# Optimization experiments

Measured on AMD Instinct MI355X. Metric: run time of the kernel, lower is better.

Reference implementation:

```python
import jax, jax.numpy as jnp
import numpy as np

B, T, H, W, C_IN = 2, 12, 80, 120, 6
F = 32  # filters
KH = KW = 3


def _conv(x, w):
    # x: (N,H,W,Cin), w: (kh,kw,Cin,Cout), SAME padding, stride 1
    return jax.lax.conv_general_dilated(
        x, w, window_strides=(1, 1), padding='SAME',
        dimension_numbers=('NHWC', 'HWIO', 'NHWC'))


def _convgru_direction(x, Wx, b, Wh_zr, Wh_h, reverse):
    """ConvGRU2D over time. x: (B,T,H,W,Cin). Returns (B,T,H,W,F)."""
    Bn, Tn, Hn, Wn, Cn = x.shape
    Fn = Wh_h.shape[-1]
    # Input convolutions for all timesteps at once (time folded into batch).
    xc = _conv(x.reshape(Bn * Tn, Hn, Wn, Cn), Wx) + b          # (B*T,H,W,3F)
    xc = xc.reshape(Bn, Tn, Hn, Wn, 3 * Fn).transpose(1, 0, 2, 3, 4)  # (T,B,H,W,3F)
    h0 = jnp.zeros((Bn, Hn, Wn, Fn), x.dtype)

    def step(h, xt):
        xz, xr, xh = jnp.split(xt, 3, axis=-1)
        hz, hr = jnp.split(_conv(h, Wh_zr), 2, axis=-1)
        z = jax.nn.sigmoid(xz + hz)              # update gate
        r = jax.nn.sigmoid(xr + hr)              # reset gate
        hh = jnp.tanh(xh + _conv(r * h, Wh_h))   # candidate state
        h_new = z * h + (1.0 - z) * hh           # keras GRU update convention
        return h_new, h_new

    _, ys = jax.lax.scan(step, h0, xc, reverse=reverse)  # ys aligned with input time order
    return ys.transpose(1, 0, 2, 3, 4)  # (B,T,H,W,F)


def setup_inputs() -> dict:
    key = jax.random.key(0)
    ks = jax.random.split(key, 9)
    sx = 1.0 / np.sqrt(KH * KW * C_IN)
    sh = 1.0 / np.sqrt(KH * KW * F)
    return {
        'x': jax.random.normal(ks[0], (B, T, H, W, C_IN), jnp.float32),
        'Wx_f': jax.random.normal(ks[1], (KH, KW, C_IN, 3 * F), jnp.float32) * sx,
        'b_f': jnp.zeros((3 * F,), jnp.float32),
        'Wh_zr_f': jax.random.normal(ks[2], (KH, KW, F, 2 * F), jnp.float32) * sh,
        'Wh_h_f': jax.random.normal(ks[3], (KH, KW, F, F), jnp.float32) * sh,
        'Wx_b': jax.random.normal(ks[4], (KH, KW, C_IN, 3 * F), jnp.float32) * sx,
        'b_b': jnp.zeros((3 * F,), jnp.float32),
        'Wh_zr_b': jax.random.normal(ks[5], (KH, KW, F, 2 * F), jnp.float32) * sh,
        'Wh_h_b': jax.random.normal(ks[6], (KH, KW, F, F), jnp.float32) * sh,
    }


def reference(x, Wx_f, b_f, Wh_zr_f, Wh_h_f, Wx_b, b_b, Wh_zr_b, Wh_h_b):
    hs_f = _convgru_direction(x, Wx_f, b_f, Wh_zr_f, Wh_h_f, reverse=False)
    hs_b = _convgru_direction(x, Wx_b, b_b, Wh_zr_b, Wh_h_b, reverse=True)
    # Bidirectional(merge_mode=None) -> concat on channel axis (module's call)
    return jnp.concatenate([hs_f, hs_b], axis=-1)  # (B,T,H,W,2F)
```

## Files before the change

### kernel.cpp

```cpp
#include <hip/hip_runtime.h>
#include <hip/hip_bf16.h>

#define Bn 2
#define Tn 12
#define Hn 80
#define Wn 120
#define CIN 6
#define SITES (Hn * Wn)
#define HSZ (4 * SITES * 32)
#define GRID 512
#define BLK 256

#define NA_D (48 * 64 * 8)
#define NB_D (24 * 64 * 8)
#define NA (2 * NA_D)
#define NB (2 * NB_D)
#define NPX (Bn * Tn * SITES)
#define PREP_TOT (NA + NB + NPX)

#define ZSTR 34

typedef __attribute__((ext_vector_type(8))) short short8;
typedef __attribute__((ext_vector_type(4))) float f32x4;

__device__ __forceinline__ short f2bf(float f) {
    union { __hip_bfloat16 h; short s; } u;
    u.h = __float2bfloat16(f);
    return u.s;
}
__device__ __forceinline__ float bf2f(short s) {
    union { float f; unsigned u; } u;
    u.u = ((unsigned)(unsigned short)s) << 16;
    return u.f;
}
__device__ __forceinline__ float fast_sigmoid(float v) {
    return __builtin_amdgcn_rcpf(1.f + __expf(-v));
}
__device__ __forceinline__ float fast_tanh(float v) {
    v = fminf(fmaxf(v, -15.f), 15.f);
    float e = __expf(2.f * v);
    return (e - 1.f) * __builtin_amdgcn_rcpf(e + 1.f);
}

__device__ __forceinline__ short8 h_load16(const short* p) {
    union { unsigned long long q[2]; short8 v; } u;
    u.q[0] = __hip_atomic_load((const unsigned long long*)p,
                               __ATOMIC_RELAXED, __HIP_MEMORY_SCOPE_AGENT);
    u.q[1] = __hip_atomic_load((const unsigned long long*)(p + 4),
                               __ATOMIC_RELAXED, __HIP_MEMORY_SCOPE_AGENT);
    return u.v;
}
__device__ __forceinline__ void h_store16(short* p, short8 v) {
    union { short8 v; unsigned long long q[2]; } u; u.v = v;
    __hip_atomic_store((unsigned long long*)p, u.q[0],
                       __ATOMIC_RELAXED, __HIP_MEMORY_SCOPE_AGENT);
    __hip_atomic_store((unsigned long long*)(p + 4), u.q[1],
                       __ATOMIC_RELAXED, __HIP_MEMORY_SCOPE_AGENT);
}

__device__ __forceinline__ int swz16(int i) { return i ^ (((i >> 5) & 7) << 3); }

__global__ __launch_bounds__(BLK) void prep_kernel(
    const float* __restrict__ Wzr_f, const float* __restrict__ Wzr_b,
    const float* __restrict__ Wh_f,  const float* __restrict__ Wh_b,
    const float* __restrict__ Wx_f,  const float* __restrict__ Wx_b,
    const float* __restrict__ x,
    short* __restrict__ bopA, short* __restrict__ bopB, short* __restrict__ xb8,
    unsigned* __restrict__ flags)
{
    int i = blockIdx.x * BLK + threadIdx.x;
    if (i < GRID) flags[i << 5] = 0;
    if (i < NA) {
        int dir = i / NA_D; int r = i % NA_D;
        int f = r / 512; int lane = (r % 512) / 8; int j = r % 8;
        int q = lane >> 4, n = lane & 15;
        int chunk = f >> 2, nt = f & 3;
        float v = 0.f;
        if (chunk < 3) {
            int tap = chunk * 4 + q;
            if (tap < 9 && j < 6) v = (dir ? Wx_b : Wx_f)[(tap * CIN + j) * 96 + nt * 16 + n];
        } else {
            int tap = chunk - 3;
            v = (dir ? Wzr_b : Wzr_f)[(tap * 32 + q * 8 + j) * 64 + nt * 16 + n];
        }
        bopA[i] = f2bf(v);
    } else if (i < NA + NB) {
        int ii = i - NA;
        int dir = ii / NB_D; int r = ii % NB_D;
        int f = r / 512; int lane = (r % 512) / 8; int j = r % 8;
        int q = lane >> 4, n = lane & 15;
        int chunk = f >> 1, ntc = f & 1;
        float v = 0.f;
        if (chunk < 3) {
            int tap = chunk * 4 + q;
            if (tap < 9 && j < 6) v = (dir ? Wx_b : Wx_f)[(tap * CIN + j) * 96 + 64 + ntc * 16 + n];
        } else {
            int tap = chunk - 3;
            v = (dir ? Wh_b : Wh_f)[(tap * 32 + q * 8 + j) * 32 + ntc * 16 + n];
        }
        bopB[ii] = f2bf(v);
    } else if (i < PREP_TOT) {
        int p = i - NA - NB;
        const float* xp = x + (size_t)p * CIN;
        short v[8];
        #pragma unroll
        for (int c = 0; c < CIN; c++) v[c] = f2bf(xp[c]);
        v[6] = 0; v[7] = 0;
        *(short8*)&xb8[(size_t)p * 8] = *(short8*)v;
    }
}

__global__ __launch_bounds__(BLK, 2) void step_all(
    const short* __restrict__ xb8,
    const short* __restrict__ bopA, const short* __restrict__ bopB,
    const float* __restrict__ b_f, const float* __restrict__ b_b,
    short* __restrict__ hb0, short* __restrict__ hb1,
    float* __restrict__ out, unsigned* __restrict__ flags)
{
    __shared__ __align__(16) short bA_l[NA_D];
    __shared__ __align__(16) short rh_l[126 * 40];
    __shared__ __align__(16) float z_l[80 * ZSTR];
    __shared__ __align__(16) short h_l[9 * 20 * 32];

    int tid = threadIdx.x, bid = blockIdx.x;
    int seg = bid & 7;
    int t1  = bid >> 3;
    int yb  = t1 & 15;
    int field = t1 >> 4;
    int dir = field >> 1, b = field & 1;
    int y0 = yb * 5, x0 = seg * 16;

    {
        const short* src = bopA + dir * NA_D;
        #pragma unroll
        for (int it = 0; it < NA_D / (BLK * 8); it++) {
            int i = (it * BLK + tid) * 8;
            *(short8*)&bA_l[i] = *(const short8*)&src[i];
        }
    }
    for (int c = tid; c < 720; c += BLK) *(short8*)&h_l[c * 8] = (short8)(short)0;

    const short* bB   = bopB + dir * NB_D;
    const float* bias = dir ? b_b : b_f;
    short* hfield0 = hb0 + (size_t)field * SITES * 32;
    short* hfield1 = hb1 + (size_t)field * SITES * 32;

    int wid = tid >> 6, lane = tid & 63;
    int n = lane & 15, q = lane >> 4, q8 = q * 8;

    unsigned* myflag = flags + (bid << 5);
    const unsigned* nflag = nullptr;
    if (tid < 8) {
        int k = tid + (tid >= 4);
        int ny = yb + k / 3 - 1, nx = seg + k % 3 - 1;
        if (ny >= 0 && ny < 16 && nx >= 0 && nx < 8)
            nflag = flags + ((unsigned)((field << 7) | (ny << 3) | nx) << 5);
    }

    int  r_gofs[2], r_lofs[2];
    bool r_img[2];
    #pragma unroll
    for (int k = 0; k < 2; k++) {
        int u = tid + k * BLK;
        r_img[k] = false; r_gofs[k] = 0; r_lofs[k] = 0;
        if (u < 400) {
            int su = u >> 2, q4 = u & 3;
            int R, C;
            if (su < 80) { int rb = su / 20; R = (rb < 2) ? rb : rb + 5; C = su % 20; }
            else { int e = su - 80; R = 2 + (e >> 2); int ci = e & 3; C = (ci < 2) ? ci : ci + 16; }
            int gy = y0 - 2 + R, gx = x0 - 2 + C;
            r_lofs[k] = swz16((R * 20 + C) * 32 + q4 * 8);
            if (gy >= 0 && gy < Hn && gx >= 0 && gx < Wn) {
                r_img[k] = true;
                r_gofs[k] = (gy * Wn + gx) * 32 + q4 * 8;
            }
        }
    }

    int hs0 = (wid * 2) * 16 + n, hs1 = hs0 + 16;
    bool av0 = hs0 < 126, av1 = hs1 < 126;
    int hr0 = hs0 / 18, hc0 = hs0 - hr0 * 18;
    int hr1 = hs1 / 18, hc1 = hs1 - hr1 * 18;
    int gy0 = y0 - 1 + hr0, gx0 = x0 - 1 + hc0;
    int gy1 = y0 - 1 + hr1, gx1 = x0 - 1 + hc1;

    int  xaofs[2][3]; bool xaok[2][3];
    #pragma unroll
    for (int c = 0; c < 3; c++) {
        int tap = c * 4 + q;
        #pragma unroll
        for (int k = 0; k < 2; k++) { xaok[k][c] = false; xaofs[k][c] = 0; }
        if (tap < 9) {
            int dy = tap / 3 - 1, dx = tap % 3 - 1;
            int ay0 = gy0 + dy, ax0 = gx0 + dx;
            int ay1 = gy1 + dy, ax1 = gx1 + dx;
            if (av0 && ay0 >= 0 && ay0 < Hn && ax0 >= 0 && ax0 < Wn) {
                xaok[0][c] = true; xaofs[0][c] = (ay0 * Wn + ax0) * 8;
            }
            if (av1 && ay1 >= 0 && ay1 < Hn && ax1 >= 0 && ax1 < Wn) {
                xaok[1][c] = true; xaofs[1][c] = (ay1 * Wn + ax1) * 8;
            }
        }
    }
    int hofs0[9], hofs1[9];
    {
        int hbase0 = ((hr0 + 1) * 20 + hc0 + 1) * 32 + q8;
        int hbase1 = ((hr1 + 1) * 20 + hc1 + 1) * 32 + q8;
        #pragma unroll
        for (int tap = 0; tap < 9; tap++) {
            int d = ((tap / 3 - 1) * 20 + (tap % 3 - 1)) * 32;
            hofs0[tap] = swz16(hbase0 + d);
            hofs1[tap] = swz16(hbase1 + d);
        }
    }

    int t0 = wid * 2;
    bool v0 = (t0 < 5), v1 = (t0 + 1 < 5);
    int tc0 = t0, tc1 = v1 ? t0 + 1 : t0;
    int yB0 = y0 + tc0, yB1 = y0 + tc1;

    int  xbofs[2][3]; bool xbok[2][3];
    #pragma unroll
    for (int c = 0; c < 3; c++) {
        int tap = c * 4 + q;
        #pragma unroll
        for (int k = 0; k < 2; k++) { xbok[k][c] = false; xbofs[k][c] = 0; }
        if (tap < 9) {
            int dy = tap / 3 - 1, dx = tap % 3 - 1;
            int ax = x0 + n + dx;
            int ay0 = yB0 + dy, ay1 = yB1 + dy;
            if (ay0 >= 0 && ay0 < Hn && ax >= 0 && ax < Wn) {
                xbok[0][c] = true; xbofs[0][c] = (ay0 * Wn + ax) * 8;
            }
            if (ay1 >= 0 && ay1 < Hn && ax >= 0 && ax < Wn) {
                xbok[1][c] = true; xbofs[1][c] = (ay1 * Wn + ax) * 8;
            }
        }
    }
    int rofs0[9], rofs1[9];
    #pragma unroll
    for (int tap = 0; tap < 9; tap++) {
        int ky = tap / 3, kx = tap % 3;
        rofs0[tap] = ((tc0 + ky) * 18 + n + kx) * 40 + q8;
        rofs1[tap] = ((tc1 + ky) * 18 + n + kx) * 40 + q8;
    }

    float bvA[4], bvB2[2];
    #pragma unroll
    for (int nt = 0; nt < 4; nt++) bvA[nt] = bias[nt * 16 + n];
    #pragma unroll
    for (int c = 0; c < 2; c++) bvB2[c] = bias[64 + c * 16 + n];

    f32x4 hst[2][2];
    #pragma unroll
    for (int a = 0; a < 2; a++)
        #pragma unroll
        for (int c = 0; c < 2; c++) hst[a][c] = (f32x4)0.f;

    float* hpub = z_l;

    __syncthreads();

    #pragma unroll 1
    for (int s = 0; s < Tn; s++) {
        int t = dir ? (Tn - 1 - s) : s;
        const short* xs   = xb8 + (size_t)((b * Tn + t) * SITES) * 8;
        const short* hbpf = (s & 1) ? hfield0 : hfield1;
        short*       hbcf = (s & 1) ? hfield1 : hfield0;

        short8 xa[2][3];
        #pragma unroll
        for (int c = 0; c < 3; c++) {
            xa[0][c] = xaok[0][c] ? *(const short8*)&xs[xaofs[0][c]] : (short8)(short)0;
            xa[1][c] = xaok[1][c] ? *(const short8*)&xs[xaofs[1][c]] : (short8)(short)0;
        }

        if (s > 0) {
            if (nflag) {
                unsigned spins = 0;
                while (__hip_atomic_load(nflag, __ATOMIC_RELAXED, __HIP_MEMORY_SCOPE_AGENT)
                       < (unsigned)s) {
                    __builtin_amdgcn_s_sleep(1);
                    if (++spins > (1u << 22)) break;
                }
            }
            __syncthreads();
        }

        short8 rv0 = (short8)(short)0, rv1 = (short8)(short)0;
        if (s > 0) {
            if (r_img[0]) rv0 = h_load16(&hbpf[r_gofs[0]]);
            if (r_img[1]) rv1 = h_load16(&hbpf[r_gofs[1]]);
        }

        f32x4 acc[2][4];
        #pragma unroll
        for (int nt = 0; nt < 4; nt++) {
            acc[0][nt] = (f32x4)bvA[nt]; acc[1][nt] = (f32x4)bvA[nt];
        }
        #pragma unroll
        for (int c = 0; c < 3; c++) {
            #pragma unroll
            for (int nt = 0; nt < 4; nt++) {
                short8 Bf = *(const short8*)&bA_l[((c * 4 + nt) * 64 + lane) * 8];
                acc[0][nt] = __builtin_amdgcn_mfma_f32_16x16x32_bf16(xa[0][c], Bf, acc[0][nt], 0, 0, 0);
                acc[1][nt] = __builtin_amdgcn_mfma_f32_16x16x32_bf16(xa[1][c], Bf, acc[1][nt], 0, 0, 0);
            }
        }

        if (s > 0) {
            if (r_img[0]) *(short8*)&h_l[r_lofs[0]] = rv0;
            if (r_img[1]) *(short8*)&h_l[r_lofs[1]] = rv1;
        }
        __syncthreads();

        if (s > 0) {
            __builtin_amdgcn_s_setprio(1);
            #pragma unroll
            for (int tap = 0; tap < 9; tap++) {
                short8 a0 = *(const short8*)&h_l[hofs0[tap]];
                short8 a1 = *(const short8*)&h_l[hofs1[tap]];
                #pragma unroll
                for (int nt = 0; nt < 4; nt++) {
                    short8 Bf = *(const short8*)&bA_l[(((tap + 3) * 4 + nt) * 64 + lane) * 8];
                    acc[0][nt] = __builtin_amdgcn_mfma_f32_16x16x32_bf16(a0, Bf, acc[0][nt], 0, 0, 0);
                    acc[1][nt] = __builtin_amdgcn_mfma_f32_16x16x32_bf16(a1, Bf, acc[1][nt], 0, 0, 0);
                }
            }
            __builtin_amdgcn_s_setprio(0);
        }

        #pragma unroll
        for (int tl = 0; tl < 2; tl++) {
            int ht = wid * 2 + tl;
            #pragma unroll
            for (int r = 0; r < 4; r++) {
                int hs_e = ht * 16 + q * 4 + r;
                if (hs_e >= 126) continue;
                int hr_e = hs_e / 18, hc_e = hs_e - hr_e * 18;
                bool inter = (hr_e >= 1 && hr_e <= 5 && hc_e >= 1 && hc_e <= 16);
                int gy_e = y0 - 1 + hr_e, gx_e = x0 - 1 + hc_e;
                bool img = (gy_e >= 0 && gy_e < Hn && gx_e >= 0 && gx_e < Wn);
                #pragma unroll
                for (int nt = 0; nt < 2; nt++) {
                    if (img && inter)
                        z_l[((hr_e - 1) * 16 + hc_e - 1) * ZSTR + nt * 16 + n] =
                            fast_sigmoid(acc[tl][nt][r]);
                }
                #pragma unroll
                for (int nt = 2; nt < 4; nt++) {
                    int ch = (nt - 2) * 16 + n;
                    float hv = bf2f(h_l[swz16(((hr_e + 1) * 20 + hc_e + 1) * 32 + ch)]);
                    float rhv = fast_sigmoid(acc[tl][nt][r]) * hv;
                    rh_l[hs_e * 40 + ch] = f2bf(rhv);
                }
            }
        }
        __syncthreads();

        f32x4 acc2[2][2];
        if (v0) {
            #pragma unroll
            for (int ntc = 0; ntc < 2; ntc++) {
                acc2[0][ntc] = (f32x4)bvB2[ntc]; acc2[1][ntc] = (f32x4)bvB2[ntc];
            }
            __builtin_amdgcn_s_setprio(1);
            #pragma unroll
            for (int chunk = 0; chunk < 12; chunk++) {
                short8 a0, a1;
                if (chunk < 3) {
                    a0 = xbok[0][chunk] ? *(const short8*)&xs[xbofs[0][chunk]] : (short8)(short)0;
                    a1 = xbok[1][chunk] ? *(const short8*)&xs[xbofs[1][chunk]] : (short8)(short)0;
                } else {
                    a0 = *(const short8*)&rh_l[rofs0[chunk - 3]];
                    a1 = *(const short8*)&rh_l[rofs1[chunk - 3]];
                }
                #pragma unroll
                for (int ntc = 0; ntc < 2; ntc++) {
                    short8 Bf = *(const short8*)&bB[((chunk * 2 + ntc) * 64 + lane) * 8];
                    acc2[0][ntc] = __builtin_amdgcn_mfma_f32_16x16x32_bf16(a0, Bf, acc2[0][ntc], 0, 0, 0);
                    acc2[1][ntc] = __builtin_amdgcn_mfma_f32_16x16x32_bf16(a1, Bf, acc2[1][ntc], 0, 0, 0);
                }
            }
            __builtin_amdgcn_s_setprio(0);
        }
        __syncthreads();

        if (v0) {
            #pragma unroll
            for (int tl = 0; tl < 2; tl++) {
                if (tl == 1 && !v1) continue;
                int ti = t0 + tl;
                #pragma unroll
                for (int ntc = 0; ntc < 2; ntc++) {
                    f32x4 hp = hst[tl][ntc];
                    f32x4 hn;
                    #pragma unroll
                    for (int r = 0; r < 4; r++) {
                        int slot = (ti * 16 + q * 4 + r) * ZSTR + ntc * 16 + n;
                        float z  = z_l[slot];
                        float hh = fast_tanh(acc2[tl][ntc][r]);
                        hn[r] = z * hp[r] + (1.f - z) * hh;
                        hpub[slot] = hn[r];
                    }
                    hst[tl][ntc] = hn;
                }
            }
        }
        __syncthreads();

        if (s + 1 < Tn) {
            #pragma unroll
            for (int j = 0; j < 2; j++) {
                int u = tid + j * BLK;
                if (u < 320) {
                    int us = u >> 2, up = u & 3;
                    int row = us >> 4, col = us & 15;
                    int gx = x0 + col;
                    if (gx < Wn) {
                        short8 hv8;
                        #pragma unroll
                        for (int e = 0; e < 8; e++)
                            hv8[e] = f2bf(hpub[us * ZSTR + up * 8 + e]);
                        *(short8*)&h_l[swz16(((row + 2) * 20 + col + 2) * 32 + up * 8)] = hv8;
                        h_store16(&hbcf[(size_t)((y0 + row) * Wn + gx) * 32 + up * 8], hv8);
                    }
                }
            }
            asm volatile("s_waitcnt vmcnt(0)" ::: "memory");
            __syncthreads();
            if (tid == 0)
                __hip_atomic_store(myflag, (unsigned)(s + 1),
                                   __ATOMIC_RELAXED, __HIP_MEMORY_SCOPE_AGENT);
        }

        {
            size_t outb = (size_t)((b * Tn + t) * SITES) * 64 + dir * 32;
            #pragma unroll
            for (int j = 0; j < 3; j++) {
                int u = tid + j * BLK;
                if (u < 640) {
                    int us = u >> 3, up = u & 7;
                    int row = us >> 4, col = us & 15;
                    int gx = x0 + col;
                    if (gx < Wn) {
                        f32x4 v;
                        #pragma unroll
                        for (int e = 0; e < 4; e++)
                            v[e] = hpub[us * ZSTR + up * 4 + e];
                        __builtin_nontemporal_store(v,
                            (f32x4*)&out[outb + (size_t)((y0 + row) * Wn + gx) * 64 + up * 4]);
                    }
                }
            }
        }
    }
}

extern "C" void kernel_launch(void* const* d_in, const int* in_sizes, int n_in,
                              void* d_out, int out_size, void* d_ws, size_t ws_size,
                              hipStream_t stream)
{
    const float* x     = (const float*)d_in[0];
    const float* Wx_f  = (const float*)d_in[1];
    const float* b_f   = (const float*)d_in[2];
    const float* Wzr_f = (const float*)d_in[3];
    const float* Wh_f  = (const float*)d_in[4];
    const float* Wx_b  = (const float*)d_in[5];
    const float* b_b   = (const float*)d_in[6];
    const float* Wzr_b = (const float*)d_in[7];
    const float* Wh_b  = (const float*)d_in[8];
    float* out = (float*)d_out;

    char* w = (char*)d_ws;
    short* hb0  = (short*)w;  w += (size_t)HSZ * 2;
    short* hb1  = (short*)w;  w += (size_t)HSZ * 2;
    short* xb8  = (short*)w;  w += (size_t)NPX * 8 * 2;
    short* bopA = (short*)w;  w += (size_t)NA * 2;
    short* bopB = (short*)w;  w += (size_t)NB * 2;
    unsigned* flags = (unsigned*)w; w += (size_t)GRID * 32 * 4;

    prep_kernel<<<(PREP_TOT + BLK - 1) / BLK, BLK, 0, stream>>>(
        Wzr_f, Wzr_b, Wh_f, Wh_b, Wx_f, Wx_b, x, bopA, bopB, xb8, flags);

    step_all<<<GRID, BLK, 0, stream>>>(xb8, bopA, bopB, b_f, b_b,
                                       hb0, hb1, out, flags);
}
```

Baseline: 219.4 us.

## Double block size so each wave handles one M-tile instead of two

The persistent step kernel now runs with 512 threads (8 waves) per block instead of 256. Each wave computes one 16-row MFMA tile rather than two, which halves per-thread accumulators and address arrays. The candidate-state update is folded into the same phase as its GEMM, removing one barrier per timestep. This gives more waves per CU to hide latency and shortens each wave's serial MFMA chain, at the cost of barriers across more waves and fewer active waves in the 5-tile candidate phase (3 of 8 idle).

```diff
diff --git a/kernel.cpp b/kernel.cpp
--- a/kernel.cpp
+++ b/kernel.cpp
@@ -9,7 +9,8 @@
 #define SITES (Hn * Wn)
 #define HSZ (4 * SITES * 32)
 #define GRID 512
-#define BLK 256
+#define BLK 512
+#define PBLK 256
 
 #define NA_D (48 * 64 * 8)
 #define NB_D (24 * 64 * 8)
@@ -60,7 +61,7 @@
 
 __device__ __forceinline__ int swz16(int i) { return i ^ (((i >> 5) & 7) << 3); }
 
-__global__ __launch_bounds__(BLK) void prep_kernel(
+__global__ __launch_bounds__(PBLK) void prep_kernel(
     const float* __restrict__ Wzr_f, const float* __restrict__ Wzr_b,
     const float* __restrict__ Wh_f,  const float* __restrict__ Wh_b,
     const float* __restrict__ Wx_f,  const float* __restrict__ Wx_b,
@@ -68,7 +69,7 @@
     short* __restrict__ bopA, short* __restrict__ bopB, short* __restrict__ xb8,
     unsigned* __restrict__ flags)
 {
-    int i = blockIdx.x * BLK + threadIdx.x;
+    int i = blockIdx.x * PBLK + threadIdx.x;
     if (i < GRID) flags[i << 5] = 0;
     if (i < NA) {
         int dir = i / NA_D; int r = i % NA_D;
@@ -110,7 +111,7 @@
     }
 }
 
-__global__ __launch_bounds__(BLK, 2) void step_all(
+__global__ __launch_bounds__(BLK, 4) void step_all(
     const short* __restrict__ xb8,
     const short* __restrict__ bopA, const short* __restrict__ bopB,
     const float* __restrict__ b_f, const float* __restrict__ b_b,
@@ -157,92 +158,70 @@
             nflag = flags + ((unsigned)((field << 7) | (ny << 3) | nx) << 5);
     }
 
-    int  r_gofs[2], r_lofs[2];
-    bool r_img[2];
-    #pragma unroll
-    for (int k = 0; k < 2; k++) {
-        int u = tid + k * BLK;
-        r_img[k] = false; r_gofs[k] = 0; r_lofs[k] = 0;
-        if (u < 400) {
-            int su = u >> 2, q4 = u & 3;
-            int R, C;
-            if (su < 80) { int rb = su / 20; R = (rb < 2) ? rb : rb + 5; C = su % 20; }
-            else { int e = su - 80; R = 2 + (e >> 2); int ci = e & 3; C = (ci < 2) ? ci : ci + 16; }
-            int gy = y0 - 2 + R, gx = x0 - 2 + C;
-            r_lofs[k] = swz16((R * 20 + C) * 32 + q4 * 8);
-            if (gy >= 0 && gy < Hn && gx >= 0 && gx < Wn) {
-                r_img[k] = true;
-                r_gofs[k] = (gy * Wn + gx) * 32 + q4 * 8;
-            }
-        }
-    }
-
-    int hs0 = (wid * 2) * 16 + n, hs1 = hs0 + 16;
-    bool av0 = hs0 < 126, av1 = hs1 < 126;
-    int hr0 = hs0 / 18, hc0 = hs0 - hr0 * 18;
-    int hr1 = hs1 / 18, hc1 = hs1 - hr1 * 18;
-    int gy0 = y0 - 1 + hr0, gx0 = x0 - 1 + hc0;
-    int gy1 = y0 - 1 + hr1, gx1 = x0 - 1 + hc1;
-
-    int  xaofs[2][3]; bool xaok[2][3];
+    int  r_gofs = 0, r_lofs = 0;
+    bool r_img = false, r_unit = (tid < 400);
+    if (r_unit) {
+        int su = tid >> 2, q4 = tid & 3;
+        int R, C;
+        if (su < 80) { int rb = su / 20; R = (rb < 2) ? rb : rb + 5; C = su % 20; }
+        else { int e = su - 80; R = 2 + (e >> 2); int ci = e & 3; C = (ci < 2) ? ci : ci + 16; }
+        int gy = y0 - 2 + R, gx = x0 - 2 + C;
+        r_lofs = swz16((R * 20 + C) * 32 + q4 * 8);
+        if (gy >= 0 && gy < Hn && gx >= 0 && gx < Wn) {
+            r_img = true;
+            r_gofs = (gy * Wn + gx) * 32 + q4 * 8;
+        }
+    }
+
+    int hs = wid * 16 + n;
+    bool av = hs < 126;
+    int hr = hs / 18, hc = hs - hr * 18;
+    int gy = y0 - 1 + hr, gx = x0 - 1 + hc;
+
+    int  xaofs[3]; bool xaok[3];
     #pragma unroll
     for (int c = 0; c < 3; c++) {
         int tap = c * 4 + q;
-        #pragma unroll
-        for (int k = 0; k < 2; k++) { xaok[k][c] = false; xaofs[k][c] = 0; }
+        xaok[c] = false; xaofs[c] = 0;
         if (tap < 9) {
             int dy = tap / 3 - 1, dx = tap % 3 - 1;
-            int ay0 = gy0 + dy, ax0 = gx0 + dx;
-            int ay1 = gy1 + dy, ax1 = gx1 + dx;
-            if (av0 && ay0 >= 0 && ay0 < Hn && ax0 >= 0 && ax0 < Wn) {
-                xaok[0][c] = true; xaofs[0][c] = (ay0 * Wn + ax0) * 8;
-            }
-            if (av1 && ay1 >= 0 && ay1 < Hn && ax1 >= 0 && ax1 < Wn) {
-                xaok[1][c] = true; xaofs[1][c] = (ay1 * Wn + ax1) * 8;
-            }
-        }
-    }
-    int hofs0[9], hofs1[9];
+            int ay = gy + dy, ax = gx + dx;
+            if (av && ay >= 0 && ay < Hn && ax >= 0 && ax < Wn) {
+                xaok[c] = true; xaofs[c] = (ay * Wn + ax) * 8;
+            }
+        }
+    }
+    int hofs[9];
     {
-        int hbase0 = ((hr0 + 1) * 20 + hc0 + 1) * 32 + q8;
-        int hbase1 = ((hr1 + 1) * 20 + hc1 + 1) * 32 + q8;
-        #pragma unroll
-        for (int tap = 0; tap < 9; tap++) {
-            int d = ((tap / 3 - 1) * 20 + (tap % 3 - 1)) * 32;
-            hofs0[tap] = swz16(hbase0 + d);
-            hofs1[tap] = swz16(hbase1 + d);
-        }
-    }
-
-    int t0 = wid * 2;
-    bool v0 = (t0 < 5), v1 = (t0 + 1 < 5);
-    int tc0 = t0, tc1 = v1 ? t0 + 1 : t0;
-    int yB0 = y0 + tc0, yB1 = y0 + tc1;
-
-    int  xbofs[2][3]; bool xbok[2][3];
+        int hbase = ((hr + 1) * 20 + hc + 1) * 32 + q8;
+        #pragma unroll
+        for (int tap = 0; tap < 9; tap++)
+            hofs[tap] = swz16(hbase + ((tap / 3 - 1) * 20 + (tap % 3 - 1)) * 32);
+    }
+
+    bool vB = (wid < 5);
+    int ti = vB ? wid : 0;
+    int yB = y0 + ti;
+
+    int  xbofs[3]; bool xbok[3];
     #pragma unroll
     for (int c = 0; c < 3; c++) {
         int tap = c * 4 + q;
-        #pragma unroll
-        for (int k = 0; k < 2; k++) { xbok[k][c] = false; xbofs[k][c] = 0; }
+        xbok[c] = false; xbofs[c] = 0;
         if (tap < 9) {
             int dy = tap / 3 - 1, dx = tap % 3 - 1;
             int ax = x0 + n + dx;
-            int ay0 = yB0 + dy, ay1 = yB1 + dy;
-            if (ay0 >= 0 && ay0 < Hn && ax >= 0 && ax < Wn) {
-                xbok[0][c] = true; xbofs[0][c] = (ay0 * Wn + ax) * 8;
-            }
-            if (ay1 >= 0 && ay1 < Hn && ax >= 0 && ax < Wn) {
-                xbok[1][c] = true; xbofs[1][c] = (ay1 * Wn + ax) * 8;
-            }
-        }
-    }
-    int rofs0[9], rofs1[9];
+            int ay = yB + dy;
+            if (ay >= 0 && ay < Hn && ax >= 0 && ax < Wn) {
+                xbok[c] = true; xbofs[c] = (ay * Wn + ax) * 8;
+            }
+        }
+    }
+    int rofs[9];
     #pragma unroll
     for (int tap = 0; tap < 9; tap++) {
         int ky = tap / 3, kx = tap % 3;
-        rofs0[tap] = ((tc0 + ky) * 18 + n + kx) * 40 + q8;
-        rofs1[tap] = ((tc1 + ky) * 18 + n + kx) * 40 + q8;
+        rofs[tap] = ((ti + ky) * 18 + n + kx) * 40 + q8;
     }
 
     float bvA[4], bvB2[2];
@@ -251,11 +230,8 @@
     #pragma unroll
     for (int c = 0; c < 2; c++) bvB2[c] = bias[64 + c * 16 + n];
 
-    f32x4 hst[2][2];
-    #pragma unroll
-    for (int a = 0; a < 2; a++)
-        #pragma unroll
-        for (int c = 0; c < 2; c++) hst[a][c] = (f32x4)0.f;
+    f32x4 hst[2];
+    hst[0] = (f32x4)0.f; hst[1] = (f32x4)0.f;
 
     float* hpub = z_l;
 
@@ -268,12 +244,10 @@
         const short* hbpf = (s & 1) ? hfield0 : hfield1;
         short*       hbcf = (s & 1) ? hfield1 : hfield0;
 
-        short8 xa[2][3];
-        #pragma unroll
-        for (int c = 0; c < 3; c++) {
-            xa[0][c] = xaok[0][c] ? *(const short8*)&xs[xaofs[0][c]] : (short8)(short)0;
-            xa[1][c] = xaok[1][c] ? *(const short8*)&xs[xaofs[1][c]] : (short8)(short)0;
-        }
+        short8 xa[3];
+        #pragma unroll
+        for (int c = 0; c < 3; c++)
+            xa[c] = xaok[c] ? *(const short8*)&xs[xaofs[c]] : (short8)(short)0;
 
         if (s > 0) {
             if (nflag) {
@@ -287,144 +261,110 @@
             __syncthreads();
         }
 
-        short8 rv0 = (short8)(short)0, rv1 = (short8)(short)0;
-        if (s > 0) {
-            if (r_img[0]) rv0 = h_load16(&hbpf[r_gofs[0]]);
-            if (r_img[1]) rv1 = h_load16(&hbpf[r_gofs[1]]);
-        }
-
-        f32x4 acc[2][4];
-        #pragma unroll
-        for (int nt = 0; nt < 4; nt++) {
-            acc[0][nt] = (f32x4)bvA[nt]; acc[1][nt] = (f32x4)bvA[nt];
-        }
+        short8 rv = (short8)(short)0;
+        if (s > 0 && r_img) rv = h_load16(&hbpf[r_gofs]);
+
+        f32x4 acc[4];
+        #pragma unroll
+        for (int nt = 0; nt < 4; nt++) acc[nt] = (f32x4)bvA[nt];
         #pragma unroll
         for (int c = 0; c < 3; c++) {
             #pragma unroll
             for (int nt = 0; nt < 4; nt++) {
                 short8 Bf = *(const short8*)&bA_l[((c * 4 + nt) * 64 + lane) * 8];
-                acc[0][nt] = __builtin_amdgcn_mfma_f32_16x16x32_bf16(xa[0][c], Bf, acc[0][nt], 0, 0, 0);
-                acc[1][nt] = __builtin_amdgcn_mfma_f32_16x16x32_bf16(xa[1][c], Bf, acc[1][nt], 0, 0, 0);
-            }
-        }
-
-        if (s > 0) {
-            if (r_img[0]) *(short8*)&h_l[r_lofs[0]] = rv0;
-            if (r_img[1]) *(short8*)&h_l[r_lofs[1]] = rv1;
-        }
+                acc[nt] = __builtin_amdgcn_mfma_f32_16x16x32_bf16(xa[c], Bf, acc[nt], 0, 0, 0);
+            }
+        }
+
+        if (s > 0 && r_img) *(short8*)&h_l[r_lofs] = rv;
         __syncthreads();
 
         if (s > 0) {
             __builtin_amdgcn_s_setprio(1);
             #pragma unroll
             for (int tap = 0; tap < 9; tap++) {
-                short8 a0 = *(const short8*)&h_l[hofs0[tap]];
-                short8 a1 = *(const short8*)&h_l[hofs1[tap]];
+                short8 a0 = *(const short8*)&h_l[hofs[tap]];
                 #pragma unroll
                 for (int nt = 0; nt < 4; nt++) {
                     short8 Bf = *(const short8*)&bA_l[(((tap + 3) * 4 + nt) * 64 + lane) * 8];
-                    acc[0][nt] = __builtin_amdgcn_mfma_f32_16x16x32_bf16(a0, Bf, acc[0][nt], 0, 0, 0);
-                    acc[1][nt] = __builtin_amdgcn_mfma_f32_16x16x32_bf16(a1, Bf, acc[1][nt], 0, 0, 0);
+                    acc[nt] = __builtin_amdgcn_mfma_f32_16x16x32_bf16(a0, Bf, acc[nt], 0, 0, 0);
                 }
             }
             __builtin_amdgcn_s_setprio(0);
         }
 
         #pragma unroll
-        for (int tl = 0; tl < 2; tl++) {
-            int ht = wid * 2 + tl;
-            #pragma unroll
-            for (int r = 0; r < 4; r++) {
-                int hs_e = ht * 16 + q * 4 + r;
-                if (hs_e >= 126) continue;
-                int hr_e = hs_e / 18, hc_e = hs_e - hr_e * 18;
-                bool inter = (hr_e >= 1 && hr_e <= 5 && hc_e >= 1 && hc_e <= 16);
-                int gy_e = y0 - 1 + hr_e, gx_e = x0 - 1 + hc_e;
-                bool img = (gy_e >= 0 && gy_e < Hn && gx_e >= 0 && gx_e < Wn);
-                #pragma unroll
-                for (int nt = 0; nt < 2; nt++) {
-                    if (img && inter)
-                        z_l[((hr_e - 1) * 16 + hc_e - 1) * ZSTR + nt * 16 + n] =
-                            fast_sigmoid(acc[tl][nt][r]);
-                }
-                #pragma unroll
-                for (int nt = 2; nt < 4; nt++) {
-                    int ch = (nt - 2) * 16 + n;
-                    float hv = bf2f(h_l[swz16(((hr_e + 1) * 20 + hc_e + 1) * 32 + ch)]);
-                    float rhv = fast_sigmoid(acc[tl][nt][r]) * hv;
-                    rh_l[hs_e * 40 + ch] = f2bf(rhv);
-                }
+        for (int r = 0; r < 4; r++) {
+            int hs_e = wid * 16 + q * 4 + r;
+            if (hs_e >= 126) continue;
+            int hr_e = hs_e / 18, hc_e = hs_e - hr_e * 18;
+            bool inter = (hr_e >= 1 && hr_e <= 5 && hc_e >= 1 && hc_e <= 16);
+            int gy_e = y0 - 1 + hr_e, gx_e = x0 - 1 + hc_e;
+            bool img = (gy_e >= 0 && gy_e < Hn && gx_e >= 0 && gx_e < Wn);
+            #pragma unroll
+            for (int nt = 0; nt < 2; nt++) {
+                if (img && inter)
+                    z_l[((hr_e - 1) * 16 + hc_e - 1) * ZSTR + nt * 16 + n] =
+                        fast_sigmoid(acc[nt][r]);
+            }
+            #pragma unroll
+            for (int nt = 2; nt < 4; nt++) {
+                int ch = (nt - 2) * 16 + n;
+                float hv = bf2f(h_l[swz16(((hr_e + 1) * 20 + hc_e + 1) * 32 + ch)]);
+                float rhv = fast_sigmoid(acc[nt][r]) * hv;
+                rh_l[hs_e * 40 + ch] = f2bf(rhv);
             }
         }
         __syncthreads();
 
-        f32x4 acc2[2][2];
-        if (v0) {
-            #pragma unroll
-            for (int ntc = 0; ntc < 2; ntc++) {
-                acc2[0][ntc] = (f32x4)bvB2[ntc]; acc2[1][ntc] = (f32x4)bvB2[ntc];
-            }
+        f32x4 acc2[2];
+        if (vB) {
+            acc2[0] = (f32x4)bvB2[0]; acc2[1] = (f32x4)bvB2[1];
             __builtin_amdgcn_s_setprio(1);
             #pragma unroll
             for (int chunk = 0; chunk < 12; chunk++) {
-                short8 a0, a1;
-                if (chunk < 3) {
-                    a0 = xbok[0][chunk] ? *(const short8*)&xs[xbofs[0][chunk]] : (short8)(short)0;
-                    a1 = xbok[1][chunk] ? *(const short8*)&xs[xbofs[1][chunk]] : (short8)(short)0;
-                } else {
-                    a0 = *(const short8*)&rh_l[rofs0[chunk - 3]];
-                    a1 = *(const short8*)&rh_l[rofs1[chunk - 3]];
-                }
+                short8 a0;
+                if (chunk < 3)
+                    a0 = xbok[chunk] ? *(const short8*)&xs[xbofs[chunk]] : (short8)(short)0;
+                else
+                    a0 = *(const short8*)&rh_l[rofs[chunk - 3]];
                 #pragma unroll
                 for (int ntc = 0; ntc < 2; ntc++) {
                     short8 Bf = *(const short8*)&bB[((chunk * 2 + ntc) * 64 + lane) * 8];
-                    acc2[0][ntc] = __builtin_amdgcn_mfma_f32_16x16x32_bf16(a0, Bf, acc2[0][ntc], 0, 0, 0);
-                    acc2[1][ntc] = __builtin_amdgcn_mfma_f32_16x16x32_bf16(a1, Bf, acc2[1][ntc], 0, 0, 0);
+                    acc2[ntc] = __builtin_amdgcn_mfma_f32_16x16x32_bf16(a0, Bf, acc2[ntc], 0, 0, 0);
                 }
             }
             __builtin_amdgcn_s_setprio(0);
+
+            #pragma unroll
+            for (int ntc = 0; ntc < 2; ntc++) {
+                f32x4 hp = hst[ntc];
+                f32x4 hn;
+                #pragma unroll
+                for (int r = 0; r < 4; r++) {
+                    int slot = (ti * 16 + q * 4 + r) * ZSTR + ntc * 16 + n;
+                    float z  = z_l[slot];
+                    float hh = fast_tanh(acc2[ntc][r]);
+                    hn[r] = z * hp[r] + (1.f - z) * hh;
+                    hpub[slot] = hn[r];
+                }
+                hst[ntc] = hn;
+            }
         }
         __syncthreads();
 
-        if (v0) {
-            #pragma unroll
-            for (int tl = 0; tl < 2; tl++) {
-                if (tl == 1 && !v1) continue;
-                int ti = t0 + tl;
-                #pragma unroll
-                for (int ntc = 0; ntc < 2; ntc++) {
-                    f32x4 hp = hst[tl][ntc];
-                    f32x4 hn;
+        if (s + 1 < Tn) {
+            if (tid < 320) {
+                int us = tid >> 2, up = tid & 3;
+                int row = us >> 4, col = us & 15;
+                int gxp = x0 + col;
+                if (gxp < Wn) {
+                    short8 hv8;
                     #pragma unroll
-                    for (int r = 0; r < 4; r++) {
-                        int slot = (ti * 16 + q * 4 + r) * ZSTR + ntc * 16 + n;
-                        float z  = z_l[slot];
-                        float hh = fast_tanh(acc2[tl][ntc][r]);
-                        hn[r] = z * hp[r] + (1.f - z) * hh;
-                        hpub[slot] = hn[r];
-                    }
-                    hst[tl][ntc] = hn;
-                }
-            }
-        }
-        __syncthreads();
-
-        if (s + 1 < Tn) {
-            #pragma unroll
-            for (int j = 0; j < 2; j++) {
-                int u = tid + j * BLK;
-                if (u < 320) {
-                    int us = u >> 2, up = u & 3;
-                    int row = us >> 4, col = us & 15;
-                    int gx = x0 + col;
-                    if (gx < Wn) {
-                        short8 hv8;
-                        #pragma unroll
-                        for (int e = 0; e < 8; e++)
-                            hv8[e] = f2bf(hpub[us * ZSTR + up * 8 + e]);
-                        *(short8*)&h_l[swz16(((row + 2) * 20 + col + 2) * 32 + up * 8)] = hv8;
-                        h_store16(&hbcf[(size_t)((y0 + row) * Wn + gx) * 32 + up * 8], hv8);
-                    }
+                    for (int e = 0; e < 8; e++)
+                        hv8[e] = f2bf(hpub[us * ZSTR + up * 8 + e]);
+                    *(short8*)&h_l[swz16(((row + 2) * 20 + col + 2) * 32 + up * 8)] = hv8;
+                    h_store16(&hbcf[(size_t)((y0 + row) * Wn + gxp) * 32 + up * 8], hv8);
                 }
             }
             asm volatile("s_waitcnt vmcnt(0)" ::: "memory");
@@ -437,19 +377,19 @@
         {
             size_t outb = (size_t)((b * Tn + t) * SITES) * 64 + dir * 32;
             #pragma unroll
-            for (int j = 0; j < 3; j++) {
+            for (int j = 0; j < 2; j++) {
                 int u = tid + j * BLK;
                 if (u < 640) {
                     int us = u >> 3, up = u & 7;
                     int row = us >> 4, col = us & 15;
-                    int gx = x0 + col;
-                    if (gx < Wn) {
+                    int gxp = x0 + col;
+                    if (gxp < Wn) {
                         f32x4 v;
                         #pragma unroll
                         for (int e = 0; e < 4; e++)
                             v[e] = hpub[us * ZSTR + up * 4 + e];
                         __builtin_nontemporal_store(v,
-                            (f32x4*)&out[outb + (size_t)((y0 + row) * Wn + gx) * 64 + up * 4]);
+                            (f32x4*)&out[outb + (size_t)((y0 + row) * Wn + gxp) * 64 + up * 4]);
                     }
                 }
             }
@@ -480,7 +420,7 @@
     short* bopB = (short*)w;  w += (size_t)NB * 2;
     unsigned* flags = (unsigned*)w; w += (size_t)GRID * 32 * 4;
 
-    prep_kernel<<<(PREP_TOT + BLK - 1) / BLK, BLK, 0, stream>>>(
+    prep_kernel<<<(PREP_TOT + PBLK - 1) / PBLK, PBLK, 0, stream>>>(
         Wzr_f, Wzr_b, Wh_f, Wh_b, Wx_f, Wx_b, x, bopA, bopB, xb8, flags);
 
     step_all<<<GRID, BLK, 0, stream>>>(xb8, bopA, bopB, b_f, b_b,
```

New measurement: 299.8 us. 1.37x slower.
